# Performance work log

Measured on AMD Instinct MI355X. Metric: run time of the kernel, lower is better.

The kernel has to match this reference:

```python
import jax, jax.numpy as jnp
import numpy as np

PAD = 0        # vocabulary.get_special_idx('pad')
VOCAB = 64     # len(vocabulary.x_vocab)
B, L, F = 64, 8192, 100


def setup_inputs() -> dict:
    key = jax.random.key(0)
    k1, k2 = jax.random.split(key)
    expression = jax.random.randint(k1, (B, L), 0, VOCAB, dtype=jnp.int32)
    sub_expression = jax.random.randint(k2, (B, F), 0, VOCAB, dtype=jnp.int32)
    return {"expression": expression, "sub_expression": sub_expression}


def reference(expression, sub_expression):
    # Original math: one-hot(expr) [B,L,V] is zero-padded with F all-zero rows,
    # then cross-correlated (grouped conv, groups==B) against one-hot(sub) with
    # pad rows zeroed. Because both sides are one-hot, the dot product over the
    # vocab axis is exactly an equality indicator, so we compute the sliding
    # match count directly without materializing one-hot tensors.
    Bb, Ll = expression.shape
    Ff = sub_expression.shape[1]
    Lp1 = Ll + 1  # number of valid conv positions: (L + F) - F + 1
    # Sentinel -1 reproduces the appended all-zero one-hot rows (matches nothing).
    expr_pad = jnp.concatenate(
        [expression, jnp.full((Bb, Ff), -1, expression.dtype)], axis=1)  # [B, L+F]

    def body(score, f):
        win = jax.lax.dynamic_slice_in_dim(expr_pad, f, Lp1, axis=1)          # [B, Lp1]
        sub_f = jax.lax.dynamic_slice_in_dim(sub_expression, f, 1, axis=1)    # [B, 1]
        match = (win == sub_f) & (sub_f != PAD)  # pad filter rows contribute 0
        return score + match.astype(jnp.float32), None

    score0 = jnp.zeros((Bb, Lp1), jnp.float32)
    score, _ = jax.lax.scan(body, score0, jnp.arange(Ff))  # [B, Lp1]

    position = jnp.argmax(score, axis=1)                 # [B]  (first max, like torch)
    max_score = jnp.max(score, axis=1, keepdims=True)    # [B, 1]
    return position, max_score
```

## Files before the change

kernel.cpp:

```cpp
#include <hip/hip_runtime.h>

#define BATCH 64
#define LEXPR 8192
#define FSUB  100
#define VOCAB 64
#define NPOS  (LEXPR + 1)
#define TPB   1024

__global__ __launch_bounds__(TPB)
void Finder_66640712565346_kernel(const int* __restrict__ expr,
                                  const int* __restrict__ sub,
                                  float* __restrict__ out) {
    __shared__ unsigned int mask[VOCAB][4];
    __shared__ unsigned int score[NPOS];
    __shared__ unsigned int red[TPB];

    const int b   = blockIdx.x;
    const int tid = threadIdx.x;

    for (int i = tid; i < VOCAB * 4; i += TPB) ((unsigned int*)mask)[i] = 0u;
    for (int i = tid; i < NPOS; i += TPB) score[i] = 0u;
    __syncthreads();

    if (tid < FSUB) {
        int v = sub[b * FSUB + tid];
        if (v != 0) atomicOr(&mask[v][tid >> 5], 1u << (tid & 31));
    }
    __syncthreads();

    const int* erow = expr + b * LEXPR;
    for (int j = tid; j < LEXPR; j += TPB) {
        int v = erow[j];
        unsigned int m0 = mask[v][0];
        unsigned int m1 = mask[v][1];
        unsigned int m2 = mask[v][2];
        unsigned int m3 = mask[v][3];
        while (m0) { int f =      __builtin_ctz(m0); m0 &= m0 - 1u; int p = j - f; if (p >= 0) atomicAdd(&score[p], 1u); }
        while (m1) { int f = 32 + __builtin_ctz(m1); m1 &= m1 - 1u; int p = j - f; if (p >= 0) atomicAdd(&score[p], 1u); }
        while (m2) { int f = 64 + __builtin_ctz(m2); m2 &= m2 - 1u; int p = j - f; if (p >= 0) atomicAdd(&score[p], 1u); }
        while (m3) { int f = 96 + __builtin_ctz(m3); m3 &= m3 - 1u; int p = j - f; if (p >= 0) atomicAdd(&score[p], 1u); }
    }
    __syncthreads();

    unsigned int best = 0u;
    for (int p = tid; p < NPOS; p += TPB) {
        unsigned int k = (score[p] << 14) | (16383u - (unsigned int)p);
        if (k > best) best = k;
    }
    red[tid] = best;
    __syncthreads();
    for (int s = TPB / 2; s > 0; s >>= 1) {
        if (tid < s) {
            unsigned int a = red[tid + s];
            if (a > red[tid]) red[tid] = a;
        }
        __syncthreads();
    }
    if (tid == 0) {
        unsigned int k = red[0];
        out[b]         = (float)(16383u - (k & 16383u));
        out[BATCH + b] = (float)(k >> 14);
    }
}

extern "C" void kernel_launch(void* const* d_in, const int* in_sizes, int n_in,
                              void* d_out, int out_size, void* d_ws, size_t ws_size,
                              hipStream_t stream) {
    const int* expr = (const int*)d_in[0];
    const int* sub  = (const int*)d_in[1];
    float* out = (float*)d_out;

    Finder_66640712565346_kernel<<<BATCH, TPB, 0, stream>>>(expr, sub, out);
}
```

Before: 65.31 us.

## Split each batch row into position segments across blocks with last-block reduction

Each batch row is now split into 8 position segments, one block each, with a 2D grid of 8x64 blocks of 256 threads instead of 64 blocks of 1024 threads. That spreads work across more CUs and shrinks the LDS score array per block. Each block reads only the expression range that can affect its segment, which adds a small halo of 99 extra elements, and finds its local best with wave shuffles. Blocks merge results through a global atomicMax, and the last block, found via a global counter, writes the outputs. The cost is a memset launch before the kernel plus global atomics and fences.

```diff
diff --git a/kernel.cpp b/kernel.cpp
--- a/kernel.cpp
+++ b/kernel.cpp
@@ -5,21 +5,30 @@
 #define FSUB  100
 #define VOCAB 64
 #define NPOS  (LEXPR + 1)
-#define TPB   1024
+#define NSEG  8
+#define SEG   1025
+#define TPB   256
 
 __global__ __launch_bounds__(TPB)
 void Finder_66640712565346_kernel(const int* __restrict__ expr,
                                   const int* __restrict__ sub,
+                                  unsigned int* __restrict__ keys,
+                                  unsigned int* __restrict__ counter,
                                   float* __restrict__ out) {
     __shared__ unsigned int mask[VOCAB][4];
-    __shared__ unsigned int score[NPOS];
-    __shared__ unsigned int red[TPB];
+    __shared__ unsigned int score[SEG];
+    __shared__ unsigned int red[TPB / 64];
+    __shared__ unsigned int is_last;
 
-    const int b   = blockIdx.x;
+    const int seg = blockIdx.x;
+    const int b   = blockIdx.y;
     const int tid = threadIdx.x;
+    const int p0  = seg * SEG;
+    const int p1  = min(p0 + SEG, NPOS);
+    const int nloc = p1 - p0;
 
     for (int i = tid; i < VOCAB * 4; i += TPB) ((unsigned int*)mask)[i] = 0u;
-    for (int i = tid; i < NPOS; i += TPB) score[i] = 0u;
+    for (int i = tid; i < SEG; i += TPB) score[i] = 0u;
     __syncthreads();
 
     if (tid < FSUB) {
@@ -28,38 +37,50 @@
     }
     __syncthreads();
 
+    const int jend = min(p1 + FSUB - 1, LEXPR);
     const int* erow = expr + b * LEXPR;
-    for (int j = tid; j < LEXPR; j += TPB) {
+    for (int j = p0 + tid; j < jend; j += TPB) {
         int v = erow[j];
         unsigned int m0 = mask[v][0];
         unsigned int m1 = mask[v][1];
         unsigned int m2 = mask[v][2];
         unsigned int m3 = mask[v][3];
-        while (m0) { int f =      __builtin_ctz(m0); m0 &= m0 - 1u; int p = j - f; if (p >= 0) atomicAdd(&score[p], 1u); }
-        while (m1) { int f = 32 + __builtin_ctz(m1); m1 &= m1 - 1u; int p = j - f; if (p >= 0) atomicAdd(&score[p], 1u); }
-        while (m2) { int f = 64 + __builtin_ctz(m2); m2 &= m2 - 1u; int p = j - f; if (p >= 0) atomicAdd(&score[p], 1u); }
-        while (m3) { int f = 96 + __builtin_ctz(m3); m3 &= m3 - 1u; int p = j - f; if (p >= 0) atomicAdd(&score[p], 1u); }
+        while (m0) { int f =      __builtin_ctz(m0); m0 &= m0 - 1u; int p = j - f; if (p >= p0 && p < p1) atomicAdd(&score[p - p0], 1u); }
+        while (m1) { int f = 32 + __builtin_ctz(m1); m1 &= m1 - 1u; int p = j - f; if (p >= p0 && p < p1) atomicAdd(&score[p - p0], 1u); }
+        while (m2) { int f = 64 + __builtin_ctz(m2); m2 &= m2 - 1u; int p = j - f; if (p >= p0 && p < p1) atomicAdd(&score[p - p0], 1u); }
+        while (m3) { int f = 96 + __builtin_ctz(m3); m3 &= m3 - 1u; int p = j - f; if (p >= p0 && p < p1) atomicAdd(&score[p - p0], 1u); }
     }
     __syncthreads();
 
     unsigned int best = 0u;
-    for (int p = tid; p < NPOS; p += TPB) {
-        unsigned int k = (score[p] << 14) | (16383u - (unsigned int)p);
+    for (int i = tid; i < nloc; i += TPB) {
+        unsigned int k = (score[i] << 14) | (16383u - (unsigned int)(p0 + i));
         if (k > best) best = k;
     }
-    red[tid] = best;
+    #pragma unroll
+    for (int off = 32; off > 0; off >>= 1) {
+        unsigned int o = __shfl_down(best, off, 64);
+        if (o > best) best = o;
+    }
+    if ((tid & 63) == 0) red[tid >> 6] = best;
     __syncthreads();
-    for (int s = TPB / 2; s > 0; s >>= 1) {
-        if (tid < s) {
-            unsigned int a = red[tid + s];
-            if (a > red[tid]) red[tid] = a;
-        }
-        __syncthreads();
+
+    if (tid == 0) {
+        unsigned int bb = red[0];
+        #pragma unroll
+        for (int w = 1; w < TPB / 64; ++w) if (red[w] > bb) bb = red[w];
+        atomicMax(&keys[b], bb);
+        __threadfence();
+        unsigned int done = atomicAdd(counter, 1u);
+        is_last = (done == (unsigned int)(NSEG * BATCH - 1)) ? 1u : 0u;
     }
-    if (tid == 0) {
-        unsigned int k = red[0];
-        out[b]         = (float)(16383u - (k & 16383u));
-        out[BATCH + b] = (float)(k >> 14);
+    __syncthreads();
+
+    if (is_last && tid < BATCH) {
+        __threadfence();
+        unsigned int k = atomicAdd(&keys[tid], 0u);
+        out[tid]         = (float)(16383u - (k & 16383u));
+        out[BATCH + tid] = (float)(k >> 14);
     }
 }
 
@@ -70,5 +91,11 @@
     const int* sub  = (const int*)d_in[1];
     float* out = (float*)d_out;
 
-    Finder_66640712565346_kernel<<<BATCH, TPB, 0, stream>>>(expr, sub, out);
+    unsigned int* keys    = (unsigned int*)d_ws;
+    unsigned int* counter = keys + BATCH;
+
+    hipMemsetAsync(d_ws, 0, (BATCH + 1) * sizeof(unsigned int), stream);
+
+    dim3 grid(NSEG, BATCH);
+    Finder_66640712565346_kernel<<<grid, TPB, 0, stream>>>(expr, sub, keys, counter, out);
 }
```

Result: slower. 72.78 us (+11.4%).
